# Performance work log

Hardware: AMD Instinct MI355X
Metric: run time of the kernel (lower is better)

The kernel has to match this reference:

```python
import jax, jax.numpy as jnp
import numpy as np

B, LQ, LKV, D = 4, 4096, 256, 1024
H, KVH, HD = 16, 4, 64
ROPE_BASE = 10000.0


def rotate_half(x):
    x1, x2 = jnp.split(x, 2, axis=-1)
    return jnp.concatenate([-x2, x1], axis=-1)


def rope_cos_sin(seq_len, dim, dtype):
    inv_freq = 1.0 / (ROPE_BASE ** (jnp.arange(0, dim, 2, dtype=jnp.float32) / dim))
    t = jnp.arange(seq_len, dtype=jnp.float32)
    freqs = t[:, None] * inv_freq[None, :]            # (T, dim/2)
    emb = jnp.concatenate([freqs, freqs], axis=-1)    # (T, dim)
    return jnp.cos(emb).astype(dtype), jnp.sin(emb).astype(dtype)


def apply_rope_indexed(x, cos, sin, pos_ids):
    # x: (B, L, H, HD); cos/sin: (T, HD); pos_ids: (L,)
    c = cos[pos_ids][None, :, None, :]
    s = sin[pos_ids][None, :, None, :]
    return x * c + rotate_half(x) * s


def setup_inputs() -> dict:
    key = jax.random.key(0)
    ks = jax.random.split(key, 10)
    sd = 1.0 / np.sqrt(D)
    return {
        "patches": jax.random.normal(ks[0], (B, LQ, D), jnp.float32),
        "latents": jax.random.normal(ks[1], (B, LKV, D), jnp.float32),
        "Wq": jax.random.normal(ks[2], (D, H * HD), jnp.float32) * sd,
        "bq": jax.random.normal(ks[3], (H * HD,), jnp.float32) * sd,
        "Wk": jax.random.normal(ks[4], (D, KVH * HD), jnp.float32) * sd,
        "bk": jax.random.normal(ks[5], (KVH * HD,), jnp.float32) * sd,
        "Wv": jax.random.normal(ks[6], (D, KVH * HD), jnp.float32) * sd,
        "bv": jax.random.normal(ks[7], (KVH * HD,), jnp.float32) * sd,
        "Wo": jax.random.normal(ks[8], (D, D), jnp.float32) * sd,
        "bo": jax.random.normal(ks[9], (D,), jnp.float32) * sd,
        "num_frames": 16,
    }


def reference(patches, latents, Wq, bq, Wk, bk, Wv, bv, Wo, bo, num_frames):
    Bc, Lq, C = patches.shape
    Lkv = latents.shape[1]
    q = (patches @ Wq + bq).reshape(Bc, Lq, H, HD)
    k = (latents @ Wk + bk).reshape(Bc, Lkv, KVH, HD)
    v = (latents @ Wv + bv).reshape(Bc, Lkv, KVH, HD)

    if num_frames > 1:
        cos, sin = rope_cos_sin(num_frames, HD, q.dtype)
        q_idx = jnp.arange(Lq) // (Lq // num_frames)
        k_idx = jnp.arange(Lkv) // (Lkv // num_frames)
        q = apply_rope_indexed(q, cos, sin, q_idx)
        k = apply_rope_indexed(k, cos, sin, k_idx)

    # GQA: expand kv heads (repeat_interleave along head axis)
    k = jnp.repeat(k, H // KVH, axis=2)
    v = jnp.repeat(v, H // KVH, axis=2)

    scale = 1.0 / np.sqrt(HD)
    scores = jnp.einsum('bqhd,bkhd->bhqk', q, k) * scale
    probs = jax.nn.softmax(scores, axis=-1)
    out = jnp.einsum('bhqk,bkhd->bqhd', probs, v).reshape(Bc, Lq, C)
    return out @ Wo + bo
```

## Files before the change

### kernel.cpp

```cpp
#include <hip/hip_runtime.h>
#include <hip/hip_fp16.h>
#include <cstdint>

typedef _Float16 f16x8 __attribute__((ext_vector_type(8)));
typedef _Float16 f16x4 __attribute__((ext_vector_type(4)));
typedef float    f32x4 __attribute__((ext_vector_type(4)));
typedef float    f32x16 __attribute__((ext_vector_type(16)));

#define MFMA16(a, b, c) __builtin_amdgcn_mfma_f32_16x16x32_f16((a), (b), (c), 0, 0, 0)
#define MFMA32(a, b, c) __builtin_amdgcn_mfma_f32_32x32x16_f16((a), (b), (c), 0, 0, 0)


__device__ __forceinline__ void async_cp16(const _Float16* g, _Float16* l) {
    __builtin_amdgcn_global_load_lds(
        (const __attribute__((address_space(1))) void*)g,
        (__attribute__((address_space(3))) void*)l, 16, 0, 0);
}

__global__ __launch_bounds__(256) void cvt_all(const float4* __restrict__ patches,
                                               const float4* __restrict__ latents,
                                               f16x4* __restrict__ p16,
                                               f16x4* __restrict__ l16) {
    const long i = (long)blockIdx.x * 256 + threadIdx.x;
    const float4 v = (i < 4194304) ? patches[i] : latents[i - 4194304];
    f16x4 o;
    o[0] = (_Float16)v.x; o[1] = (_Float16)v.y;
    o[2] = (_Float16)v.z; o[3] = (_Float16)v.w;
    if (i < 4194304) p16[i] = o; else l16[i - 4194304] = o;
}

__global__ __launch_bounds__(256) void transpose_all(
    const float* __restrict__ Wq, const float* __restrict__ Wk,
    const float* __restrict__ Wv, const float* __restrict__ Wo,
    _Float16* __restrict__ WqT, _Float16* __restrict__ WkvT,
    _Float16* __restrict__ WoT) {
    const int z = blockIdx.z;
    const float* W;
    _Float16* WT;
    int Nd;
    if (z == 0)      { W = Wq; WT = WqT;                       Nd = 1024; }
    else if (z == 1) { W = Wk; WT = WkvT;                      Nd = 256;  }
    else if (z == 2) { W = Wv; WT = WkvT + (size_t)256 * 1024; Nd = 256;  }
    else             { W = Wo; WT = WoT;                       Nd = 1024; }
    const int n0 = blockIdx.x * 64, k0 = blockIdx.y * 64;
    if (n0 >= Nd) return;

    __shared__ float T[64][65];
    const int tid = threadIdx.x;
    const int nl = tid & 63, kg = tid >> 6;
#pragma unroll
    for (int i = 0; i < 16; ++i) {
        const int kl = kg * 16 + i;
        T[kl][nl] = W[(size_t)(k0 + kl) * Nd + n0 + nl];
    }
    __syncthreads();
    const int kl = tid & 63;
#pragma unroll
    for (int i = 0; i < 16; ++i) {
        const int nl2 = kg * 16 + i;
        WT[(size_t)(n0 + nl2) * 1024 + k0 + kl] = (_Float16)T[kl][nl2];
    }
}

__global__ void catbias(const float* __restrict__ a, const float* __restrict__ b,
                        float* __restrict__ o) {
    const int i = threadIdx.x;
    o[i] = (i < 256) ? a[i] : b[i - 256];
}

template <int EPI>
__global__ __launch_bounds__(256, 2) void gemm32(const _Float16* __restrict__ A,
                                                 const _Float16* __restrict__ BT,
                                                 const float* __restrict__ bias,
                                                 void* __restrict__ Cp,
                                                 const int* __restrict__ nfp) {
    constexpr int K = 1024;
    __shared__ _Float16 As[256 * 64];
    __shared__ _Float16 Bs[128 * 64];

    const int tid = threadIdx.x;
    const int lane = tid & 63, l31 = lane & 31, hh = lane >> 5;
    const int w = tid >> 6, wm = w >> 1, wn = w & 1;

    const int n0 = blockIdx.x * 128;
    const int m0 = blockIdx.y * 256;

    f32x16 acc[4][2];
#pragma unroll
    for (int mt = 0; mt < 4; ++mt)
#pragma unroll
        for (int nt = 0; nt < 2; ++nt)
#pragma unroll
            for (int v = 0; v < 16; ++v) acc[mt][nt][v] = 0.f;

    for (int k0 = 0; k0 < K; k0 += 64) {
#pragma unroll
        for (int i = 0; i < 8; ++i) {
            const int id = i * 256 + tid;
            const int r = id >> 3;
            const int c = (id & 7) ^ (r & 7);
            async_cp16(A + (size_t)(m0 + r) * K + k0 + c * 8,
                       As + i * 2048 + w * 512);
        }
#pragma unroll
        for (int i = 0; i < 4; ++i) {
            const int id = i * 256 + tid;
            const int r = id >> 3;
            const int c = (id & 7) ^ (r & 7);
            async_cp16(BT + (size_t)(n0 + r) * K + k0 + c * 8,
                       Bs + i * 2048 + w * 512);
        }
        __syncthreads();

#pragma unroll
        for (int kk = 0; kk < 4; ++kk) {
            f16x8 af[4], bf[2];
#pragma unroll
            for (int mt = 0; mt < 4; ++mt) {
                const int row = wm * 128 + mt * 32 + l31;
                const int pc = (kk * 2 + hh) ^ (row & 7);
                af[mt] = *(const f16x8*)&As[row * 64 + pc * 8];
            }
#pragma unroll
            for (int nt = 0; nt < 2; ++nt) {
                const int row = wn * 64 + nt * 32 + l31;
                const int pc = (kk * 2 + hh) ^ (row & 7);
                bf[nt] = *(const f16x8*)&Bs[row * 64 + pc * 8];
            }
#pragma unroll
            for (int mt = 0; mt < 4; ++mt)
#pragma unroll
                for (int nt = 0; nt < 2; ++nt)
                    acc[mt][nt] = MFMA32(af[mt], bf[nt], acc[mt][nt]);
        }
        __syncthreads();
    }

    const int nf = nfp[0];
    const int nbase = n0 + wn * 64;

    float bb[2];
#pragma unroll
    for (int nt = 0; nt < 2; ++nt) bb[nt] = bias[nbase + nt * 32 + l31];
#pragma unroll
    for (int mt = 0; mt < 4; ++mt)
#pragma unroll
        for (int nt = 0; nt < 2; ++nt)
#pragma unroll
            for (int v = 0; v < 16; ++v) acc[mt][nt][v] += bb[nt];

    {
        _Float16* kout = (_Float16*)Cp;
        _Float16* vout = kout + (size_t)4 * 4 * 256 * 64;
        if (nbase < 256) {
            const float l2b = 13.287712379549449f;
            const float inv = exp2f(-((float)l31 * (1.0f / 32.0f)) * l2b);
            const int dv = 256 / (nf > 1 ? nf : 1);
            const int kvh = nbase >> 6;
#pragma unroll
            for (int mt = 0; mt < 4; ++mt) {
#pragma unroll
                for (int v = 0; v < 16; ++v) {
                    const int m = m0 + wm * 128 + mt * 32 + (v & 3) + 8 * (v >> 2) + 4 * hh;
                    const int b = m >> 8, lkv = m & 255;
                    if (nf > 1) {
                        const int pos = lkv / dv;
                        float s, c;
                        __sincosf((float)pos * inv, &s, &c);
                        const float x1 = acc[mt][0][v], x2 = acc[mt][1][v];
                        acc[mt][0][v] = x1 * c - x2 * s;
                        acc[mt][1][v] = x2 * c + x1 * s;
                    }
#pragma unroll
                    for (int nt = 0; nt < 2; ++nt) {
                        const int hd = nt * 32 + l31;
                        kout[(((size_t)(b * 4 + kvh)) * 256 + lkv) * 64 + hd] =
                            (_Float16)acc[mt][nt][v];
                    }
                }
            }
        } else {
            const int kvh = (nbase - 256) >> 6;
#pragma unroll
            for (int mt = 0; mt < 4; ++mt) {
#pragma unroll
                for (int v = 0; v < 16; ++v) {
                    const int m = m0 + wm * 128 + mt * 32 + (v & 3) + 8 * (v >> 2) + 4 * hh;
                    const int b = m >> 8, lkv = m & 255;
                    const int s = (lkv & 0xE0) | ((lkv & 12) << 1) |
                                  ((lkv & 16) >> 2) | (lkv & 3);
#pragma unroll
                    for (int nt = 0; nt < 2; ++nt) {
                        const int hd = nt * 32 + l31;
                        vout[(((size_t)(b * 4 + kvh)) * 64 + hd) * 256 + s] =
                            (_Float16)acc[mt][nt][v];
                    }
                }
            }
        }
    }
}

template <int EPI>
__global__ __launch_bounds__(512, 2) void gemm8p(const _Float16* __restrict__ A,
                                                 const _Float16* __restrict__ BT,
                                                 const float* __restrict__ bias,
                                                 void* __restrict__ Cp,
                                                 const int* __restrict__ nfp) {
    constexpr int K = 1024;
    __shared__ alignas(16) _Float16 lds[2][2][2][128 * 64];

    const int tid = threadIdx.x;
    const int lane = tid & 63, quad = lane >> 4, l15 = lane & 15;
    const int w = tid >> 6, wm = w >> 2, wn = w & 3;

    int lin = blockIdx.x;
    lin = (lin & 7) * 32 + (lin >> 3);
    const int m0 = (lin >> 2) * 256;
    const int n0 = (lin & 3) * 256;

    f32x4 acc[8][4];
#pragma unroll
    for (int mf = 0; mf < 8; ++mf)
#pragma unroll
        for (int nf = 0; nf < 4; ++nf)
#pragma unroll
            for (int rr = 0; rr < 4; ++rr) acc[mf][nf][rr] = 0.f;

    f16x8 ra[4][2], rb[4][2];

#define STAGE(BUF, MAT, HALF, KK0)                                              \
    {                                                                           \
        const _Float16* g_ = (MAT) ? BT : A;                                    \
        const int rb_ = ((MAT) ? n0 : m0) + (HALF) * 128;                       \
        _Float16* dst_ = &lds[BUF][MAT][HALF][0];                               \
        _Pragma("unroll") for (int i_ = 0; i_ < 2; ++i_) {                      \
            const int id_ = i_ * 512 + tid;                                     \
            const int r_ = id_ >> 3;                                            \
            const int c_ = (id_ & 7) ^ (r_ & 7);                                \
            async_cp16(g_ + (size_t)(rb_ + r_) * K + (KK0) + c_ * 8,            \
                       dst_ + i_ * 4096 + w * 512);                             \
        }                                                                       \
    }

#define LDA4(BUF, MH)                                                           \
    _Pragma("unroll") for (int i_ = 0; i_ < 4; ++i_)                            \
    _Pragma("unroll") for (int ks_ = 0; ks_ < 2; ++ks_) {                       \
        const int row_ = ((MH) * 4 + i_) * 16 + l15;                            \
        ra[i_][ks_] = *(const f16x8*)&lds[BUF][0][wm]                           \
            [row_ * 64 + (((ks_ * 4 + quad) ^ (l15 & 7)) * 8)];                 \
    }

#define LDB2(BUF, NFROM)                                                        \
    _Pragma("unroll") for (int j_ = 0; j_ < 2; ++j_)                            \
    _Pragma("unroll") for (int ks_ = 0; ks_ < 2; ++ks_) {                       \
        const int nf_ = (NFROM) + j_;                                           \
        const int row_ = (wn & 1) * 64 + nf_ * 16 + l15;                        \
        rb[nf_][ks_] = *(const f16x8*)&lds[BUF][1][wn >> 1]                     \
            [row_ * 64 + (((ks_ * 4 + quad) ^ (l15 & 7)) * 8)];                 \
    }

#define QUAD(QM, QN)                                                            \
    {                                                                           \
        __builtin_amdgcn_s_setprio(1);                                          \
        _Pragma("unroll") for (int i_ = 0; i_ < 4; ++i_)                        \
        _Pragma("unroll") for (int j_ = 0; j_ < 2; ++j_)                        \
        _Pragma("unroll") for (int ks_ = 0; ks_ < 2; ++ks_)                     \
            acc[(QM) * 4 + i_][(QN) * 2 + j_] =                                 \
                MFMA16(ra[i_][ks_], rb[(QN) * 2 + j_][ks_],                     \
                       acc[(QM) * 4 + i_][(QN) * 2 + j_]);                      \
        __builtin_amdgcn_s_setprio(0);                                          \
    }

#define FENCE() asm volatile("" ::: "memory")
#define BARR()  FENCE(); __builtin_amdgcn_s_barrier(); FENCE()
#define LGKM0() asm volatile("s_waitcnt lgkmcnt(0)" ::: "memory");              \
                __builtin_amdgcn_sched_barrier(0)
#define VMC4()  asm volatile("s_waitcnt vmcnt(4)" ::: "memory")

    STAGE(0, 1, 0, 0);
    STAGE(0, 1, 1, 0);
    STAGE(0, 0, 0, 0);
    STAGE(0, 0, 1, 0);
    STAGE(1, 1, 0, 64);
    STAGE(1, 0, 0, 64);
    VMC4();
    BARR();

    int k0 = 0;
#pragma unroll 1
    for (int it = 0; it < 8; ++it) {
        const int k_t1 = k0 + 64;
        const int k_n0 = (k0 + 128 < K) ? k0 + 128 : K - 64;
        const int k_n1 = (k0 + 192 < K) ? k0 + 192 : K - 64;
        LDA4(0, 0); LDB2(0, 0);
        STAGE(1, 1, 1, k_t1);
        BARR(); LGKM0(); QUAD(0, 0); BARR();
        LDB2(0, 2);
        STAGE(1, 0, 1, k_t1);
        BARR(); LGKM0(); QUAD(0, 1); BARR();
        LDA4(0, 1);
        STAGE(0, 1, 0, k_n0);
        BARR(); LGKM0(); QUAD(1, 0); BARR();
        STAGE(0, 1, 1, k_n0);
        BARR(); LGKM0(); QUAD(1, 1); VMC4(); BARR();
        LDA4(1, 0); LDB2(1, 0);
        STAGE(0, 0, 0, k_n0);
        BARR(); LGKM0(); QUAD(0, 0); BARR();
        LDB2(1, 2);
        STAGE(0, 0, 1, k_n0);
        BARR(); LGKM0(); QUAD(0, 1); BARR();
        LDA4(1, 1);
        STAGE(1, 1, 0, k_n1);
        BARR(); LGKM0(); QUAD(1, 0); BARR();
        STAGE(1, 0, 0, k_n1);
        BARR(); LGKM0(); QUAD(1, 1); VMC4(); BARR();
        k0 += 128;
    }
    asm volatile("s_waitcnt vmcnt(0)" ::: "memory");

    const int nf_frames = nfp[0];
    float bb[4];
#pragma unroll
    for (int nf = 0; nf < 4; ++nf) bb[nf] = bias[n0 + wn * 64 + nf * 16 + l15];
#pragma unroll
    for (int mf = 0; mf < 8; ++mf)
#pragma unroll
        for (int nf = 0; nf < 4; ++nf)
#pragma unroll
            for (int rr = 0; rr < 4; ++rr) acc[mf][nf][rr] += bb[nf];

    if constexpr (EPI == 0) {
        const float l2b = 13.287712379549449f;
        const float inv0 = exp2f(-((float)l15 * (1.0f / 32.0f)) * l2b);
        const float inv1 = exp2f(-((float)(16 + l15) * (1.0f / 32.0f)) * l2b);
        const int dv = 4096 / (nf_frames > 1 ? nf_frames : 1);
        _Float16* O = (_Float16*)Cp;
        const int head = (n0 + wn * 64) >> 6;
#pragma unroll
        for (int mf = 0; mf < 8; ++mf) {
#pragma unroll
            for (int rr = 0; rr < 4; ++rr) {
                const int m = m0 + wm * 128 + mf * 16 + quad * 4 + rr;
                const int b = m >> 12, lq = m & 4095;
                if (nf_frames > 1) {
                    const int pos = lq / dv;
                    float s0, c0, s1, c1;
                    __sincosf((float)pos * inv0, &s0, &c0);
                    __sincosf((float)pos * inv1, &s1, &c1);
                    const float x0 = acc[mf][0][rr], x2 = acc[mf][2][rr];
                    const float x1 = acc[mf][1][rr], x3 = acc[mf][3][rr];
                    acc[mf][0][rr] = x0 * c0 - x2 * s0;
                    acc[mf][2][rr] = x2 * c0 + x0 * s0;
                    acc[mf][1][rr] = x1 * c1 - x3 * s1;
                    acc[mf][3][rr] = x3 * c1 + x1 * s1;
                }
                const size_t base = (((size_t)(b * 16 + head)) * 4096 + lq) * 64;
#pragma unroll
                for (int nf = 0; nf < 4; ++nf)
                    O[base + nf * 16 + l15] = (_Float16)(acc[mf][nf][rr] * 0.125f);
            }
        }
    } else {
        float* O = (float*)Cp;
#pragma unroll
        for (int mf = 0; mf < 8; ++mf) {
#pragma unroll
            for (int rr = 0; rr < 4; ++rr) {
                const int m = m0 + wm * 128 + mf * 16 + quad * 4 + rr;
#pragma unroll
                for (int nf = 0; nf < 4; ++nf)
                    O[(size_t)m * 1024 + n0 + wn * 64 + nf * 16 + l15] =
                        acc[mf][nf][rr];
            }
        }
    }
#undef STAGE
#undef LDA4
#undef LDB2
#undef QUAD
#undef FENCE
#undef BARR
#undef LGKM0
#undef VMC4
}

__global__ __launch_bounds__(512, 4) void attn5(const _Float16* __restrict__ qh,
                                                const _Float16* __restrict__ kh,
                                                const _Float16* __restrict__ vp,
                                                _Float16* __restrict__ attn) {
    __shared__ _Float16 Ks[256 * 64];
    __shared__ _Float16 Vs[64 * 256];

    const int tid = threadIdx.x;
    const int w = tid >> 6, lane = tid & 63, quad = lane >> 4, l15 = lane & 15;
    const int bh = blockIdx.x, b = bh >> 4, h = bh & 15, kvh = h >> 2;
    const int q0 = blockIdx.y * 512;

    const _Float16* kb = kh + (size_t)(b * 4 + kvh) * 256 * 64;
    const _Float16* vb = vp + (size_t)(b * 4 + kvh) * 64 * 256;
    const _Float16* qb = qh + ((size_t)bh * 4096 + q0) * 64;

#pragma unroll
    for (int i = 0; i < 4; ++i) {
        const int id = i * 512 + tid;
        const int r = id >> 3;
        const int c = (id & 7) ^ (r & 7);
        async_cp16(kb + (size_t)r * 64 + c * 8, Ks + i * 4096 + w * 512);
    }
#pragma unroll
    for (int i = 0; i < 4; ++i) {
        const int id = i * 512 + tid;
        const int hd = id >> 5;
        const int s5 = id & 31;
        const int c = s5 ^ ((hd & 7) << 2);
        async_cp16(vb + (size_t)hd * 256 + c * 8, Vs + i * 4096 + w * 512);
    }
    __syncthreads();

    const int sw = l15 & 7;
    const int p0 = quad ^ sw;
    const int vsw = sw << 2;
    const int crot = w & 3;

    const _Float16* qpre = qb + (size_t)(w * 64 + crot * 16 + l15) * 64 + quad * 8;
    f16x8 bq0 = *(const f16x8*)qpre;
    f16x8 bq1 = *(const f16x8*)(qpre + 32);

#pragma unroll 1
    for (int cc = 0; cc < 4; ++cc) {
        const int chunk = (cc + crot) & 3;
        const int qrow = w * 64 + chunk * 16;

        const int nchunk = (cc + 1 + crot) & 3;
        const _Float16* np = qb + (size_t)(w * 64 + nchunk * 16 + l15) * 64 + quad * 8;
        const f16x8 nq0 = *(const f16x8*)np;
        const f16x8 nq1 = *(const f16x8*)(np + 32);

        f32x4 st[16];
#pragma unroll
        for (int t = 0; t < 16; ++t)
#pragma unroll
            for (int rr = 0; rr < 4; ++rr) st[t][rr] = 0.f;

#pragma unroll
        for (int t = 0; t < 16; ++t) {
            const int row = t * 16 + l15;
            const f16x8 ka0 = *(const f16x8*)&Ks[row * 64 + p0 * 8];
            const f16x8 ka1 = *(const f16x8*)&Ks[row * 64 + (p0 ^ 4) * 8];
            st[t] = MFMA16(ka0, bq0, st[t]);
            st[t] = MFMA16(ka1, bq1, st[t]);
        }

        float rm = -1e30f;
#pragma unroll
        for (int t = 0; t < 16; ++t)
#pragma unroll
            for (int rr = 0; rr < 4; ++rr) rm = fmaxf(rm, st[t][rr]);
        rm = fmaxf(rm, __shfl_xor(rm, 16, 64));
        rm = fmaxf(rm, __shfl_xor(rm, 32, 64));

        float rs = 0.f;
#pragma unroll
        for (int t = 0; t < 16; ++t) {
#pragma unroll
            for (int rr = 0; rr < 4; ++rr) {
                st[t][rr] = __expf(st[t][rr] - rm);
                rs += st[t][rr];
            }
        }
        rs += __shfl_xor(rs, 16, 64);
        rs += __shfl_xor(rs, 32, 64);
        const float ir = 1.0f / rs;

        int vo = 0;
        asm volatile("" : "+v"(vo));

        f32x4 o[4];
#pragma unroll
        for (int nt = 0; nt < 4; ++nt)
#pragma unroll
            for (int rr = 0; rr < 4; ++rr) o[nt][rr] = 0.f;

#pragma unroll
        for (int c = 0; c < 8; ++c) {
            f16x8 pb;
#pragma unroll
            for (int j = 0; j < 8; ++j)
                pb[j] = (_Float16)st[2 * c + (j >> 2)][j & 3];
#pragma unroll
            for (int nt = 0; nt < 4; ++nt) {
                const f16x8 va = *(const f16x8*)&Vs[(nt * 16 + l15) * 256 +
                                                   (((c * 4 + quad) ^ vsw) * 8) + vo];
                o[nt] = MFMA16(va, pb, o[nt]);
            }
        }

        const size_t rowbase = ((size_t)b * 4096 + q0 + qrow + l15) * 1024 + h * 64;
#pragma unroll
        for (int nt = 0; nt < 4; ++nt) {
            f16x4 ov;
#pragma unroll
            for (int rr = 0; rr < 4; ++rr) ov[rr] = (_Float16)(o[nt][rr] * ir);
            *(f16x4*)&attn[rowbase + nt * 16 + quad * 4] = ov;
        }

        bq0 = nq0; bq1 = nq1;
    }
}

extern "C" void kernel_launch(void* const* d_in, const int* in_sizes, int n_in,
                              void* d_out, int out_size, void* d_ws, size_t ws_size,
                              hipStream_t stream) {
    const float* patches = (const float*)d_in[0];
    const float* latents = (const float*)d_in[1];
    const float* Wq = (const float*)d_in[2];
    const float* bq = (const float*)d_in[3];
    const float* Wk = (const float*)d_in[4];
    const float* bk = (const float*)d_in[5];
    const float* Wv = (const float*)d_in[6];
    const float* bv = (const float*)d_in[7];
    const float* Wo = (const float*)d_in[8];
    const float* bo = (const float*)d_in[9];
    const int*   nf = (const int*)d_in[10];
    float* out = (float*)d_out;
    (void)in_sizes; (void)n_in; (void)out_size; (void)ws_size;

    char* p = (char*)d_ws;
    _Float16* WqT  = (_Float16*)p; p += (size_t)1024 * 1024 * 2;
    _Float16* WkvT = (_Float16*)p; p += (size_t)512 * 1024 * 2;
    _Float16* WoT  = (_Float16*)p; p += (size_t)1024 * 1024 * 2;
    float*    bkv  = (float*)p;    p += 4096;
    _Float16* p16  = (_Float16*)p; p += (size_t)4 * 4096 * 1024 * 2;
    _Float16* l16  = (_Float16*)p; p += (size_t)4 * 256 * 1024 * 2;
    _Float16* q_h  = (_Float16*)p; p += (size_t)4 * 16 * 4096 * 64 * 2;
    _Float16* k_h  = (_Float16*)p; p += (size_t)4 * 4 * 256 * 64 * 2;
    _Float16* v_pi = (_Float16*)p; p += (size_t)4 * 4 * 256 * 64 * 2;
    _Float16* attn_h = (_Float16*)p; p += (size_t)16384 * 1024 * 2;

    cvt_all<<<17408, 256, 0, stream>>>((const float4*)patches, (const float4*)latents,
                                       (f16x4*)p16, (f16x4*)l16);
    transpose_all<<<dim3(16, 16, 4), 256, 0, stream>>>(Wq, Wk, Wv, Wo, WqT, WkvT, WoT);
    catbias<<<1, 512, 0, stream>>>(bk, bv, bkv);

    gemm32<1><<<dim3(4, 4), 256, 0, stream>>>(l16, WkvT, bkv, k_h, nf);
    gemm8p<0><<<256, 512, 0, stream>>>(p16, WqT, bq, q_h, nf);

    attn5<<<dim3(64, 8), 512, 0, stream>>>(q_h, k_h, v_pi, attn_h);

    gemm8p<2><<<256, 512, 0, stream>>>(attn_h, WoT, bo, out, nf);
}
```

Before: 284.6 us.

## Fuse prep kernels, hoist RoPE sincos, use exp2 softmax with MFMA row sums

```diff
diff --git a/kernel.cpp b/kernel.cpp
--- a/kernel.cpp
+++ b/kernel.cpp
@@ -4,6 +4,7 @@
 
 typedef _Float16 f16x8 __attribute__((ext_vector_type(8)));
 typedef _Float16 f16x4 __attribute__((ext_vector_type(4)));
+typedef __fp16   fp16x2 __attribute__((ext_vector_type(2)));
 typedef float    f32x4 __attribute__((ext_vector_type(4)));
 typedef float    f32x16 __attribute__((ext_vector_type(16)));
 
@@ -17,24 +18,35 @@
         (__attribute__((address_space(3))) void*)l, 16, 0, 0);
 }
 
-__global__ __launch_bounds__(256) void cvt_all(const float4* __restrict__ patches,
-                                               const float4* __restrict__ latents,
-                                               f16x4* __restrict__ p16,
-                                               f16x4* __restrict__ l16) {
-    const long i = (long)blockIdx.x * 256 + threadIdx.x;
-    const float4 v = (i < 4194304) ? patches[i] : latents[i - 4194304];
-    f16x4 o;
-    o[0] = (_Float16)v.x; o[1] = (_Float16)v.y;
-    o[2] = (_Float16)v.z; o[3] = (_Float16)v.w;
-    if (i < 4194304) p16[i] = o; else l16[i - 4194304] = o;
-}
-
-__global__ __launch_bounds__(256) void transpose_all(
+__global__ __launch_bounds__(256) void prep(
+    const float4* __restrict__ patches, const float4* __restrict__ latents,
+    f16x4* __restrict__ p16, f16x4* __restrict__ l16,
     const float* __restrict__ Wq, const float* __restrict__ Wk,
     const float* __restrict__ Wv, const float* __restrict__ Wo,
     _Float16* __restrict__ WqT, _Float16* __restrict__ WkvT,
-    _Float16* __restrict__ WoT) {
-    const int z = blockIdx.z;
+    _Float16* __restrict__ WoT,
+    const float* __restrict__ bk, const float* __restrict__ bv,
+    float* __restrict__ bkv) {
+    __shared__ float T[64][65];
+    const int tid = threadIdx.x;
+    const int bid = blockIdx.x;
+
+    if (bid < 17408) {
+        const long i = (long)bid * 256 + tid;
+        const float4 v = (i < 4194304) ? patches[i] : latents[i - 4194304];
+        f16x4 o;
+        o[0] = (_Float16)v.x; o[1] = (_Float16)v.y;
+        o[2] = (_Float16)v.z; o[3] = (_Float16)v.w;
+        if (i < 4194304) p16[i] = o; else l16[i - 4194304] = o;
+        return;
+    }
+    if (bid == 18432) {
+        bkv[tid] = bk[tid];
+        bkv[256 + tid] = bv[tid];
+        return;
+    }
+    const int t = bid - 17408;
+    const int z = t >> 8, rem = t & 255, xb = rem & 15, yb = rem >> 4;
     const float* W;
     _Float16* WT;
     int Nd;
@@ -42,11 +54,9 @@
     else if (z == 1) { W = Wk; WT = WkvT;                      Nd = 256;  }
     else if (z == 2) { W = Wv; WT = WkvT + (size_t)256 * 1024; Nd = 256;  }
     else             { W = Wo; WT = WoT;                       Nd = 1024; }
-    const int n0 = blockIdx.x * 64, k0 = blockIdx.y * 64;
+    const int n0 = xb * 64, k0 = yb * 64;
     if (n0 >= Nd) return;
 
-    __shared__ float T[64][65];
-    const int tid = threadIdx.x;
     const int nl = tid & 63, kg = tid >> 6;
 #pragma unroll
     for (int i = 0; i < 16; ++i) {
@@ -60,12 +70,6 @@
         const int nl2 = kg * 16 + i;
         WT[(size_t)(n0 + nl2) * 1024 + k0 + kl] = (_Float16)T[kl][nl2];
     }
-}
-
-__global__ void catbias(const float* __restrict__ a, const float* __restrict__ b,
-                        float* __restrict__ o) {
-    const int i = threadIdx.x;
-    o[i] = (i < 256) ? a[i] : b[i - 256];
 }
 
 template <int EPI>
@@ -331,12 +335,25 @@
             for (int rr = 0; rr < 4; ++rr) acc[mf][nf][rr] += bb[nf];
 
     if constexpr (EPI == 0) {
+        const float SCALE = 0.18033688011112042f;
         const float l2b = 13.287712379549449f;
         const float inv0 = exp2f(-((float)l15 * (1.0f / 32.0f)) * l2b);
         const float inv1 = exp2f(-((float)(16 + l15) * (1.0f / 32.0f)) * l2b);
-        const int dv = 4096 / (nf_frames > 1 ? nf_frames : 1);
         _Float16* O = (_Float16*)Cp;
         const int head = (n0 + wn * 64) >> 6;
+        int dv = 4096;
+        bool uni = false;
+        float us0 = 0.f, uc0 = 1.f, us1 = 0.f, uc1 = 1.f;
+        if (nf_frames > 1) {
+            dv = 4096 / nf_frames;
+            const int lqb = (m0 + wm * 128) & 4095;
+            uni = (lqb / dv) == ((lqb + 127) / dv);
+            if (uni) {
+                const float fp = (float)(lqb / dv);
+                __sincosf(fp * inv0, &us0, &uc0);
+                __sincosf(fp * inv1, &us1, &uc1);
+            }
+        }
 #pragma unroll
         for (int mf = 0; mf < 8; ++mf) {
 #pragma unroll
@@ -344,10 +361,14 @@
                 const int m = m0 + wm * 128 + mf * 16 + quad * 4 + rr;
                 const int b = m >> 12, lq = m & 4095;
                 if (nf_frames > 1) {
-                    const int pos = lq / dv;
                     float s0, c0, s1, c1;
-                    __sincosf((float)pos * inv0, &s0, &c0);
-                    __sincosf((float)pos * inv1, &s1, &c1);
+                    if (uni) {
+                        s0 = us0; c0 = uc0; s1 = us1; c1 = uc1;
+                    } else {
+                        const int pos = lq / dv;
+                        __sincosf((float)pos * inv0, &s0, &c0);
+                        __sincosf((float)pos * inv1, &s1, &c1);
+                    }
                     const float x0 = acc[mf][0][rr], x2 = acc[mf][2][rr];
                     const float x1 = acc[mf][1][rr], x3 = acc[mf][3][rr];
                     acc[mf][0][rr] = x0 * c0 - x2 * s0;
@@ -358,7 +379,7 @@
                 const size_t base = (((size_t)(b * 16 + head)) * 4096 + lq) * 64;
 #pragma unroll
                 for (int nf = 0; nf < 4; ++nf)
-                    O[base + nf * 16 + l15] = (_Float16)(acc[mf][nf][rr] * 0.125f);
+                    O[base + nf * 16 + l15] = (_Float16)(acc[mf][nf][rr] * SCALE);
             }
         }
     } else {
@@ -423,6 +444,10 @@
     const int vsw = sw << 2;
     const int crot = w & 3;
 
+    f16x8 ones;
+#pragma unroll
+    for (int j = 0; j < 8; ++j) ones[j] = (_Float16)1.0f;
+
     const _Float16* qpre = qb + (size_t)(w * 64 + crot * 16 + l15) * 64 + quad * 8;
     f16x8 bq0 = *(const f16x8*)qpre;
     f16x8 bq1 = *(const f16x8*)(qpre + 32);
@@ -452,26 +477,24 @@
             st[t] = MFMA16(ka1, bq1, st[t]);
         }
 
-        float rm = -1e30f;
+        float tm[16];
 #pragma unroll
         for (int t = 0; t < 16; ++t)
-#pragma unroll
-            for (int rr = 0; rr < 4; ++rr) rm = fmaxf(rm, st[t][rr]);
+            tm[t] = fmaxf(fmaxf(fmaxf(st[t][0], st[t][1]), st[t][2]), st[t][3]);
+        const float a0 = fmaxf(fmaxf(tm[0], tm[1]), tm[2]);
+        const float a1 = fmaxf(fmaxf(tm[3], tm[4]), tm[5]);
+        const float a2 = fmaxf(fmaxf(tm[6], tm[7]), tm[8]);
+        const float a3 = fmaxf(fmaxf(tm[9], tm[10]), tm[11]);
+        const float a4 = fmaxf(fmaxf(tm[12], tm[13]), tm[14]);
+        float rm = fmaxf(fmaxf(fmaxf(a0, a1), a2), fmaxf(fmaxf(a3, a4), tm[15]));
         rm = fmaxf(rm, __shfl_xor(rm, 16, 64));
         rm = fmaxf(rm, __shfl_xor(rm, 32, 64));
 
-        float rs = 0.f;
-#pragma unroll
-        for (int t = 0; t < 16; ++t) {
-#pragma unroll
-            for (int rr = 0; rr < 4; ++rr) {
-                st[t][rr] = __expf(st[t][rr] - rm);
-                rs += st[t][rr];
-            }
-        }
-        rs += __shfl_xor(rs, 16, 64);
-        rs += __shfl_xor(rs, 32, 64);
-        const float ir = 1.0f / rs;
+#pragma unroll
+        for (int t = 0; t < 16; ++t)
+#pragma unroll
+            for (int rr = 0; rr < 4; ++rr)
+                st[t][rr] = exp2f(st[t][rr] - rm);
 
         int vo = 0;
         asm volatile("" : "+v"(vo));
@@ -481,13 +504,19 @@
         for (int nt = 0; nt < 4; ++nt)
 #pragma unroll
             for (int rr = 0; rr < 4; ++rr) o[nt][rr] = 0.f;
+        f32x4 osum;
+#pragma unroll
+        for (int rr = 0; rr < 4; ++rr) osum[rr] = 0.f;
 
 #pragma unroll
         for (int c = 0; c < 8; ++c) {
-            f16x8 pb;
-#pragma unroll
-            for (int j = 0; j < 8; ++j)
-                pb[j] = (_Float16)st[2 * c + (j >> 2)][j & 3];
+            union { fp16x2 h2[4]; f16x8 v; } pbu;
+            pbu.h2[0] = __builtin_amdgcn_cvt_pkrtz(st[2 * c][0], st[2 * c][1]);
+            pbu.h2[1] = __builtin_amdgcn_cvt_pkrtz(st[2 * c][2], st[2 * c][3]);
+            pbu.h2[2] = __builtin_amdgcn_cvt_pkrtz(st[2 * c + 1][0], st[2 * c + 1][1]);
+            pbu.h2[3] = __builtin_amdgcn_cvt_pkrtz(st[2 * c + 1][2], st[2 * c + 1][3]);
+            const f16x8 pb = pbu.v;
+            osum = MFMA16(ones, pb, osum);
 #pragma unroll
             for (int nt = 0; nt < 4; ++nt) {
                 const f16x8 va = *(const f16x8*)&Vs[(nt * 16 + l15) * 256 +
@@ -495,6 +524,8 @@
                 o[nt] = MFMA16(va, pb, o[nt]);
             }
         }
+
+        const float ir = 1.0f / osum[0];
 
         const size_t rowbase = ((size_t)b * 4096 + q0 + qrow + l15) * 1024 + h * 64;
 #pragma unroll
@@ -538,10 +569,9 @@
     _Float16* v_pi = (_Float16*)p; p += (size_t)4 * 4 * 256 * 64 * 2;
     _Float16* attn_h = (_Float16*)p; p += (size_t)16384 * 1024 * 2;
 
-    cvt_all<<<17408, 256, 0, stream>>>((const float4*)patches, (const float4*)latents,
-                                       (f16x4*)p16, (f16x4*)l16);
-    transpose_all<<<dim3(16, 16, 4), 256, 0, stream>>>(Wq, Wk, Wv, Wo, WqT, WkvT, WoT);
-    catbias<<<1, 512, 0, stream>>>(bk, bv, bkv);
+    prep<<<18433, 256, 0, stream>>>((const float4*)patches, (const float4*)latents,
+                                    (f16x4*)p16, (f16x4*)l16,
+                                    Wq, Wk, Wv, Wo, WqT, WkvT, WoT, bk, bv, bkv);
 
     gemm32<1><<<dim3(4, 4), 256, 0, stream>>>(l16, WkvT, bkv, k_h, nf);
     gemm8p<0><<<256, 512, 0, stream>>>(p16, WqT, bq, q_h, nf);
```

New measurement: 284.0 us. Within noise of the previous version (-0.2%).
